# Kernel tuning notes

Measured on AMD Instinct MI355X. Metric: run time of the kernel, lower is better.

Reference implementation:

```python
import jax, jax.numpy as jnp
import numpy as np

N_HEAD = 16
N_FEAT = 1024
D_K = N_FEAT // N_HEAD
BATCH = 8
SEQ = 1024
LN_EPS = 1e-5
MIN_VAL = float(np.finfo(np.float32).min)


def setup_inputs() -> dict:
    key = jax.random.key(0)
    ks = jax.random.split(key, 8)
    s = 0.02  # small init scale for weights to keep activations sane
    return {
        "x": jax.random.normal(ks[0], (BATCH, SEQ, N_FEAT), jnp.float32),
        "pos_k": jax.random.normal(ks[1], (SEQ, SEQ, D_K), jnp.float32) * s,
        "mask": jnp.ones((BATCH, SEQ, SEQ), jnp.int32),
        "ln_scale": jnp.ones((N_FEAT,), jnp.float32),
        "ln_bias": jnp.zeros((N_FEAT,), jnp.float32),
        "wq": jax.random.normal(ks[2], (N_FEAT, N_FEAT), jnp.float32) * s,
        "bq": jnp.zeros((N_FEAT,), jnp.float32),
        "wk": jax.random.normal(ks[3], (N_FEAT, N_FEAT), jnp.float32) * s,
        "bk": jnp.zeros((N_FEAT,), jnp.float32),
        "wv": jax.random.normal(ks[4], (N_FEAT, N_FEAT), jnp.float32) * s,
        "bv": jnp.zeros((N_FEAT,), jnp.float32),
        "wo": jax.random.normal(ks[5], (N_FEAT, N_FEAT), jnp.float32) * s,
        "bo": jnp.zeros((N_FEAT,), jnp.float32),
    }


def reference(x, pos_k, mask, ln_scale, ln_bias, wq, bq, wk, bk, wv, bv, wo, bo):
    b, t, f = x.shape
    h, d = N_HEAD, D_K
    # LayerNorm over feature dim
    mu = jnp.mean(x, axis=-1, keepdims=True)
    var = jnp.mean((x - mu) ** 2, axis=-1, keepdims=True)
    xn = (x - mu) / jnp.sqrt(var + LN_EPS) * ln_scale + ln_bias
    # QKV projections (torch Linear: y = x @ W^T + b), split heads -> (b, h, t, d)
    q = (xn @ wq.T + bq).reshape(b, t, h, d).transpose(0, 2, 1, 3)
    k = (xn @ wk.T + bk).reshape(b, t, h, d).transpose(0, 2, 1, 3)
    v = (xn @ wv.T + bv).reshape(b, t, h, d).transpose(0, 2, 1, 3)
    # content score A and relative-position score B
    A = jnp.einsum("bhtd,bhsd->bhts", q, k)
    B = jnp.einsum("bhtd,tsd->bhts", q, pos_k)
    scores = (A + B) / jnp.sqrt(jnp.asarray(d, scores_dtype := x.dtype))
    m = (mask[:, None, :, :] == 0)  # (b, 1, t, s) broadcast over heads
    scores = jnp.where(m, MIN_VAL, scores)
    attn = jax.nn.softmax(scores, axis=-1)
    attn = jnp.where(m, 0.0, attn)
    out = jnp.einsum("bhts,bhsd->bhtd", attn, v)
    out = out.transpose(0, 2, 1, 3).reshape(b, t, h * d)
    return out @ wo.T + bo
```

## Files before the change

kernel.cpp:

```cpp
#include <hip/hip_runtime.h>
#include <hip/hip_bf16.h>

typedef unsigned short ushort_t;
typedef short short8 __attribute__((ext_vector_type(8)));
typedef unsigned short ushort8 __attribute__((ext_vector_type(8)));
typedef unsigned short ushortx4 __attribute__((ext_vector_type(4)));
typedef float fx4 __attribute__((ext_vector_type(4)));
typedef int ix4 __attribute__((ext_vector_type(4)));

#define MFMA(a, b, c) __builtin_amdgcn_mfma_f32_16x16x32_bf16((a), (b), (c), 0, 0, 0)

__device__ __forceinline__ ushort_t f2bf(float f) {
  __hip_bfloat16 h = __float2bfloat16(f);
  return *(ushort_t*)&h;
}
__device__ __forceinline__ float bf2f(ushort_t h) {
  union { unsigned u; float f; } c; c.u = ((unsigned)h) << 16;
  return c.f;
}
__device__ __forceinline__ void gload16(const ushort_t* g, ushort_t* l) {
  __builtin_amdgcn_global_load_lds((const __attribute__((address_space(1))) void*)g,
                                   (__attribute__((address_space(3))) void*)l, 16, 0, 0);
}

__global__ __launch_bounds__(256) void cvt4_kernel(const float* __restrict__ s0,
                                                   const float* __restrict__ s1,
                                                   const float* __restrict__ s2,
                                                   const float* __restrict__ s3,
                                                   ushort_t* __restrict__ d0,
                                                   ushort_t* __restrict__ d1,
                                                   ushort_t* __restrict__ d2,
                                                   ushort_t* __restrict__ d3) {
  int bi = blockIdx.x;
  const float* src = (bi < 1024) ? s0 : (bi < 2048) ? s1 : (bi < 3072) ? s2 : s3;
  ushort_t* dst = (bi < 1024) ? d0 : (bi < 2048) ? d1 : (bi < 3072) ? d2 : d3;
  int i = (bi & 1023) * 256 + threadIdx.x;
  fx4 v = *(const fx4*)&src[(size_t)i * 4];
  ushortx4 o;
#pragma unroll
  for (int j = 0; j < 4; ++j) o[j] = f2bf(v[j]);
  *(ushortx4*)&dst[(size_t)i * 4] = o;
}

__global__ __launch_bounds__(256) void ln_kernel(const float* __restrict__ x,
                                                 const float* __restrict__ sc,
                                                 const float* __restrict__ bi,
                                                 ushort_t* __restrict__ xn) {
  __shared__ float red[8];
  int row = blockIdx.x, tid = threadIdx.x;
  const float* xr = x + (size_t)row * 1024;
  fx4 v = *(const fx4*)&xr[tid * 4];
  float s = v[0] + v[1] + v[2] + v[3];
  float s2 = v[0] * v[0] + v[1] * v[1] + v[2] * v[2] + v[3] * v[3];
#pragma unroll
  for (int m = 32; m >= 1; m >>= 1) {
    s += __shfl_xor(s, m);
    s2 += __shfl_xor(s2, m);
  }
  int wave = tid >> 6;
  if ((tid & 63) == 0) { red[wave * 2] = s; red[wave * 2 + 1] = s2; }
  __syncthreads();
  s = red[0] + red[2] + red[4] + red[6];
  s2 = red[1] + red[3] + red[5] + red[7];
  float mu = s * (1.f / 1024.f);
  float var = s2 * (1.f / 1024.f) - mu * mu;
  float rs = rsqrtf(var + 1e-5f);
  fx4 scv = *(const fx4*)&sc[tid * 4];
  fx4 biv = *(const fx4*)&bi[tid * 4];
  ushortx4 o;
#pragma unroll
  for (int j = 0; j < 4; ++j) o[j] = f2bf((v[j] - mu) * rs * scv[j] + biv[j]);
  *(ushortx4*)&xn[(size_t)row * 1024 + tid * 4] = o;
}

__global__ __launch_bounds__(256) void maskpack_kernel(const int* __restrict__ mask,
                                                       unsigned* __restrict__ bits) {
  __shared__ unsigned char nib[256];
  int row = blockIdx.x, tid = threadIdx.x;
  ix4 m = *(const ix4*)&mask[(size_t)row * 1024 + tid * 4];
  nib[tid] = (unsigned char)((m[0] != 0 ? 1 : 0) | (m[1] != 0 ? 2 : 0) |
                             (m[2] != 0 ? 4 : 0) | (m[3] != 0 ? 8 : 0));
  __syncthreads();
  if (tid < 32) {
    unsigned w = 0;
#pragma unroll
    for (int j = 0; j < 8; ++j) w |= ((unsigned)nib[tid * 8 + j]) << (j * 4);
    bits[(size_t)row * 32 + tid] = w;
  }
}

template <int F32OUT>
__global__ __launch_bounds__(256) void gemm_bt(const ushort_t* __restrict__ A,
                                               const ushort_t* __restrict__ B,
                                               const float* __restrict__ bias, void* C,
                                               int M, int N, int K) {
  __shared__ ushort_t lA[4096];
  __shared__ ushort_t lB[4096];
  int bm = blockIdx.y * 128, bn = blockIdx.x * 128;
  int tid = threadIdx.x;
  int wave = tid >> 6, lane = tid & 63;
  int wm = (wave >> 1) * 64, wn = (wave & 1) * 64;
  int l15 = lane & 15, lg = lane >> 4;
  int r0 = tid >> 2, c0 = (tid & 3) * 8;
  int g1 = 256 + tid, r1 = g1 >> 2, c1 = (g1 & 3) * 8;
  int lb0 = (wave * 64) * 8;
  int lb1 = (256 + wave * 64) * 8;
  fx4 acc[4][4] = {};
  for (int k0 = 0; k0 < K; k0 += 32) {
    __syncthreads();
    gload16(&A[(size_t)(bm + r0) * K + k0 + c0], &lA[lb0]);
    gload16(&A[(size_t)(bm + r1) * K + k0 + c1], &lA[lb1]);
    gload16(&B[(size_t)(bn + r0) * K + k0 + c0], &lB[lb0]);
    gload16(&B[(size_t)(bn + r1) * K + k0 + c1], &lB[lb1]);
    __syncthreads();
    short8 af[4], bf[4];
#pragma unroll
    for (int i = 0; i < 4; ++i) af[i] = *(const short8*)&lA[(wm + i * 16 + l15) * 32 + lg * 8];
#pragma unroll
    for (int i = 0; i < 4; ++i) bf[i] = *(const short8*)&lB[(wn + i * 16 + l15) * 32 + lg * 8];
#pragma unroll
    for (int i = 0; i < 4; ++i)
#pragma unroll
      for (int j = 0; j < 4; ++j) acc[i][j] = MFMA(af[i], bf[j], acc[i][j]);
  }
#pragma unroll
  for (int j = 0; j < 4; ++j) {
    int n = bn + wn + j * 16 + l15;
    float bv = bias[n];
#pragma unroll
    for (int i = 0; i < 4; ++i) {
      int mr = bm + wm + i * 16 + lg * 4;
#pragma unroll
      for (int r = 0; r < 4; ++r) {
        float val = acc[i][j][r] + bv;
        if (F32OUT)
          ((float*)C)[(size_t)(mr + r) * N + n] = val;
        else
          ((ushort_t*)C)[(size_t)(mr + r) * N + n] = f2bf(val);
      }
    }
  }
}

__device__ __forceinline__ void loadset(const float* base, int c, fx4* r) {
  const float* p = base + (size_t)c * 1024;
  r[0] = *(const fx4*)p;
  r[1] = *(const fx4*)(p + 4);
  r[2] = *(const fx4*)(p + 32);
  r[3] = *(const fx4*)(p + 36);
}
__device__ __forceinline__ void cvtset(const fx4* r, short8& f0, short8& f1) {
#pragma unroll
  for (int j = 0; j < 4; ++j) {
    f0[j] = (short)f2bf(r[0][j]); f0[j + 4] = (short)f2bf(r[1][j]);
    f1[j] = (short)f2bf(r[2][j]); f1[j + 4] = (short)f2bf(r[3][j]);
  }
}

__global__ __launch_bounds__(256, 3) void ball_kernel(const ushort_t* __restrict__ q,
                                                      const float* __restrict__ pos_k,
                                                      ushort_t* __restrict__ B_all) {
  __shared__ ushort_t lq[128 * 64];
  int t = blockIdx.y, sx = blockIdx.x;
  int tid = threadIdx.x, wave = tid >> 6, lane = tid & 63, l15 = lane & 15, lg = lane >> 4;
  const float* pk = pos_k + (size_t)t * 65536;
  int sw = sx * 512 + wave * 128;
  const float* base = pk + (size_t)(sw + l15) * 64 + lg * 8;

  fx4 raw[4][4];
#pragma unroll
  for (int c = 0; c < 4; ++c) loadset(base, c, raw[c]);

#pragma unroll
  for (int it = 0; it < 4; ++it) {
    int u = tid + it * 256;
    int row = u >> 3, cu = u & 7;
    ushort8 vv = *(const ushort8*)&q[((size_t)((row >> 4) * 1024 + t)) * 1024 + (row & 15) * 64 + cu * 8];
    *(ushort8*)&lq[(row * 128 + ((cu * 16) ^ ((row & 7) << 4))) >> 1] = vv;
  }
  __syncthreads();

  short8 af0[4], af1[4];
#pragma unroll
  for (int c = 0; c < 4; ++c) cvtset(raw[c], af0[c], af1[c]);

#pragma unroll
  for (int g = 0; g < 2; ++g) {
    if (g == 0) {
#pragma unroll
      for (int c = 0; c < 4; ++c) loadset(base, 4 + c, raw[c]);
    }
    __builtin_amdgcn_sched_barrier(0);
#pragma unroll
    for (int j = 0; j < 8; ++j) {
      int row_ = j * 16 + l15;
      int cb_ = (row_ & 7) << 4;
      short8 q0 = *(const short8*)&lq[(row_ * 128 + ((lg * 16) ^ cb_)) >> 1];
      short8 q1 = *(const short8*)&lq[(row_ * 128 + ((64 + lg * 16) ^ cb_)) >> 1];
      fx4 z = {};
      size_t rb = ((size_t)row_ << 20) + (size_t)t * 1024 + (size_t)(sw + g * 64);
#pragma unroll
      for (int c = 0; c < 4; ++c) {
        fx4 a = MFMA(af0[c], q0, z);
        a = MFMA(af1[c], q1, a);
        ushortx4 o;
#pragma unroll
        for (int r = 0; r < 4; ++r) o[r] = f2bf(a[r]);
        *(ushortx4*)&B_all[rb + c * 16 + lg * 4] = o;
      }
    }
    __builtin_amdgcn_sched_barrier(0);
    if (g == 0) {
#pragma unroll
      for (int c = 0; c < 4; ++c) cvtset(raw[c], af0[c], af1[c]);
    }
  }
}

__global__ __launch_bounds__(256) void attn_kernel(const ushort_t* __restrict__ q,
                                                   const ushort_t* __restrict__ k,
                                                   const ushort_t* __restrict__ v,
                                                   const ushort_t* __restrict__ B_all,
                                                   const unsigned* __restrict__ mbits,
                                                   ushort_t* __restrict__ out) {
  __shared__ ushort_t lK[64][72];
  __shared__ ushort_t lVt[64][72];
  __shared__ ushort_t lP[4][16][72];
  int bh = blockIdx.y, b = bh >> 4, h = bh & 15;
  int t0 = blockIdx.x * 64;
  int tid = threadIdx.x, wave = tid >> 6, lane = tid & 63, l15 = lane & 15, lg = lane >> 4;
  int tw = t0 + wave * 16;
  short8 qf[2];
#pragma unroll
  for (int ks = 0; ks < 2; ++ks)
    qf[ks] = *(const short8*)&q[((size_t)(b * 1024 + tw + l15)) * 1024 + h * 64 + ks * 32 + lg * 8];
  fx4 o[4] = {};
  float mrun = -INFINITY, lsum = 0.f;
  int trow = tw + l15;
  const unsigned* mrow = &mbits[((size_t)b * 1024 + trow) * 32];
  size_t ballrow = ((size_t)bh * 1024 + trow) * 1024;

  int rs = tid >> 3, c8g = tid & 7, c8 = c8g * 8;
  const ushort_t* kbase = &k[((size_t)(b * 1024) + rs) * 1024 + h * 64 + c8];
  const ushort_t* vbase = &v[((size_t)(b * 1024) + rs) * 1024 + h * 64 + c8];
  ushort8 kr0 = *(const ushort8*)(kbase);
  ushort8 kr1 = *(const ushort8*)(kbase + 32 * 1024);
  ushort8 vr0 = *(const ushort8*)(vbase);
  ushort8 vr1 = *(const ushort8*)(vbase + 32 * 1024);
  int vs0 = (rs + 8 * c8g) & 63;
  int vs1 = (rs + 32 + 8 * c8g) & 63;

  for (int s0 = 0; s0 < 1024; s0 += 64) {
    __syncthreads();
    *(ushort8*)&lK[rs][c8] = kr0;
    *(ushort8*)&lK[rs + 32][c8] = kr1;
#pragma unroll
    for (int j = 0; j < 8; ++j) {
      lVt[c8 + j][vs0] = vr0[j];
      lVt[c8 + j][vs1] = vr1[j];
    }
    __syncthreads();
    if (s0 + 64 < 1024) {
      size_t off = (size_t)(s0 + 64) * 1024;
      kr0 = *(const ushort8*)(kbase + off);
      kr1 = *(const ushort8*)(kbase + off + 32 * 1024);
      vr0 = *(const ushort8*)(vbase + off);
      vr1 = *(const ushort8*)(vbase + off + 32 * 1024);
    }
    __builtin_amdgcn_sched_barrier(0);
    ushortx4 b4[4];
#pragma unroll
    for (int mf = 0; mf < 4; ++mf)
      b4[mf] = *(const ushortx4*)&B_all[ballrow + s0 + mf * 16 + lg * 4];
    uint2 mw = *(const uint2*)&mrow[s0 >> 5];
    unsigned long long wb = ((unsigned long long)mw.y << 32) | mw.x;
    __builtin_amdgcn_sched_barrier(0);
    fx4 st[4];
#pragma unroll
    for (int mf = 0; mf < 4; ++mf) {
      fx4 c4 = {};
#pragma unroll
      for (int ks = 0; ks < 2; ++ks) {
        short8 kf = *(const short8*)&lK[mf * 16 + l15][ks * 32 + lg * 8];
        c4 = MFMA(kf, qf[ks], c4);
      }
      st[mf] = c4;
    }
    float p[16];
    float mt = -INFINITY;
#pragma unroll
    for (int mf = 0; mf < 4; ++mf) {
#pragma unroll
      for (int r = 0; r < 4; ++r) {
        float sv = (st[mf][r] + bf2f(b4[mf][r])) * 0.125f;
        int sl = mf * 16 + lg * 4 + r;
        if (!((wb >> sl) & 1ull)) sv = -INFINITY;
        p[mf * 4 + r] = sv;
        mt = fmaxf(mt, sv);
      }
    }
    mt = fmaxf(mt, __shfl_xor(mt, 16));
    mt = fmaxf(mt, __shfl_xor(mt, 32));
    float mnew = fmaxf(mrun, mt);
    float alpha = (mnew == -INFINITY) ? 1.f : __expf(mrun - mnew);
    mrun = mnew;
    float ps = 0.f;
#pragma unroll
    for (int i = 0; i < 16; ++i) {
      float pv = (mnew == -INFINITY) ? 0.f : __expf(p[i] - mnew);
      p[i] = pv;
      ps += pv;
    }
    ps += __shfl_xor(ps, 16);
    ps += __shfl_xor(ps, 32);
    lsum = lsum * alpha + ps;
#pragma unroll
    for (int mf = 0; mf < 4; ++mf) {
      ushortx4 pk4;
#pragma unroll
      for (int r = 0; r < 4; ++r) pk4[r] = f2bf(p[mf * 4 + r]);
      *(ushortx4*)&lP[wave][l15][mf * 16 + lg * 4] = pk4;
    }
    float aw[4];
#pragma unroll
    for (int r = 0; r < 4; ++r) aw[r] = __shfl(alpha, lg * 4 + r);
#pragma unroll
    for (int nf = 0; nf < 4; ++nf)
#pragma unroll
      for (int r = 0; r < 4; ++r) o[nf][r] *= aw[r];
#pragma unroll
    for (int ks = 0; ks < 2; ++ks) {
      short8 pf = *(const short8*)&lP[wave][l15][ks * 32 + lg * 8];
#pragma unroll
      for (int nf = 0; nf < 4; ++nf) {
        int d_ = nf * 16 + l15;
        int sb_ = (ks * 32 + lg * 8 + 8 * (d_ >> 3)) & 63;
        short8 vf = *(const short8*)&lVt[d_][sb_];
        o[nf] = MFMA(pf, vf, o[nf]);
      }
    }
  }
  float rl = (lsum > 0.f) ? 1.f / lsum : 0.f;
  float rw[4];
#pragma unroll
  for (int r = 0; r < 4; ++r) rw[r] = __shfl(rl, lg * 4 + r);
#pragma unroll
  for (int nf = 0; nf < 4; ++nf)
#pragma unroll
    for (int r = 0; r < 4; ++r) {
      float val = o[nf][r] * rw[r];
      out[((size_t)(b * 1024 + tw + lg * 4 + r)) * 1024 + h * 64 + nf * 16 + l15] = f2bf(val);
    }
}

extern "C" void kernel_launch(void* const* d_in, const int* in_sizes, int n_in, void* d_out,
                              int out_size, void* d_ws, size_t ws_size, hipStream_t stream) {
  (void)in_sizes; (void)n_in; (void)out_size; (void)ws_size;
  const float* x = (const float*)d_in[0];
  const float* pos_k = (const float*)d_in[1];
  const int* mask = (const int*)d_in[2];
  const float* ln_scale = (const float*)d_in[3];
  const float* ln_bias = (const float*)d_in[4];
  const float* wq = (const float*)d_in[5];
  const float* bq = (const float*)d_in[6];
  const float* wk = (const float*)d_in[7];
  const float* bk = (const float*)d_in[8];
  const float* wv = (const float*)d_in[9];
  const float* bv = (const float*)d_in[10];
  const float* wo = (const float*)d_in[11];
  const float* bo = (const float*)d_in[12];
  float* out = (float*)d_out;
  char* ws = (char*)d_ws;
  const size_t MB = 1ull << 20;
  ushort_t* xn = (ushort_t*)(ws + 0 * MB);
  ushort_t* qb = (ushort_t*)(ws + 16 * MB);
  ushort_t* kb = (ushort_t*)(ws + 32 * MB);
  ushort_t* vb = (ushort_t*)(ws + 48 * MB);
  ushort_t* ao = (ushort_t*)(ws + 64 * MB);
  ushort_t* wqb = (ushort_t*)(ws + 80 * MB);
  ushort_t* wkb = (ushort_t*)(ws + 82 * MB);
  ushort_t* wvb = (ushort_t*)(ws + 84 * MB);
  ushort_t* wob = (ushort_t*)(ws + 86 * MB);
  ushort_t* ball = (ushort_t*)(ws + 88 * MB);
  unsigned* mbits = (unsigned*)(ws + 0 * MB);

  cvt4_kernel<<<4096, 256, 0, stream>>>(wq, wk, wv, wo, wqb, wkb, wvb, wob);
  ln_kernel<<<8192, 256, 0, stream>>>(x, ln_scale, ln_bias, xn);
  dim3 gg(8, 64);
  gemm_bt<0><<<gg, 256, 0, stream>>>(xn, wqb, bq, qb, 8192, 1024, 1024);
  gemm_bt<0><<<gg, 256, 0, stream>>>(xn, wkb, bk, kb, 8192, 1024, 1024);
  gemm_bt<0><<<gg, 256, 0, stream>>>(xn, wvb, bv, vb, 8192, 1024, 1024);
  maskpack_kernel<<<8192, 256, 0, stream>>>(mask, mbits);
  ball_kernel<<<dim3(2, 1024), 256, 0, stream>>>(qb, pos_k, ball);
  attn_kernel<<<dim3(16, 128), 256, 0, stream>>>(qb, kb, vb, ball, mbits, ao);
  gemm_bt<1><<<gg, 256, 0, stream>>>(ao, wob, bo, out, 8192, 1024, 1024);
}
```

Measured before the change: 436.1 us.

## Fold softmax scale into Q projection, use exp2, skip mask and rescale when possible

Q is pre-scaled in the projection epilogue by 1/sqrt(d)*log2(e), so attention scores feed exp2 directly and the per-element scale multiply disappears. Because ball is built from the scaled q, the positional term carries the same scale. Masking is skipped when the whole wave's tile is unmasked, and the online-softmax rescale of the output accumulators is skipped when the running max did not grow. V transpose stores pack two values per 32-bit write, the P tile in LDS uses an XOR swizzle instead of padding, and K/V pointers advance incrementally. The extra wave votes add branches, and bf16 rounding of pre-scaled q slightly changes numerics.

```diff
diff --git a/kernel.cpp b/kernel.cpp
--- a/kernel.cpp
+++ b/kernel.cpp
@@ -7,8 +7,11 @@
 typedef unsigned short ushortx4 __attribute__((ext_vector_type(4)));
 typedef float fx4 __attribute__((ext_vector_type(4)));
 typedef int ix4 __attribute__((ext_vector_type(4)));
+typedef unsigned uint2v __attribute__((ext_vector_type(2)));
 
 #define MFMA(a, b, c) __builtin_amdgcn_mfma_f32_16x16x32_bf16((a), (b), (c), 0, 0, 0)
+
+#define QSCALE 0.18033688011112042f
 
 __device__ __forceinline__ ushort_t f2bf(float f) {
   __hip_bfloat16 h = __float2bfloat16(f);
@@ -93,7 +96,7 @@
 __global__ __launch_bounds__(256) void gemm_bt(const ushort_t* __restrict__ A,
                                                const ushort_t* __restrict__ B,
                                                const float* __restrict__ bias, void* C,
-                                               int M, int N, int K) {
+                                               int M, int N, int K, float oscale) {
   __shared__ ushort_t lA[4096];
   __shared__ ushort_t lB[4096];
   int bm = blockIdx.y * 128, bn = blockIdx.x * 128;
@@ -132,7 +135,7 @@
       int mr = bm + wm + i * 16 + lg * 4;
 #pragma unroll
       for (int r = 0; r < 4; ++r) {
-        float val = acc[i][j][r] + bv;
+        float val = (acc[i][j][r] + bv) * oscale;
         if (F32OUT)
           ((float*)C)[(size_t)(mr + r) * N + n] = val;
         else
@@ -224,8 +227,8 @@
                                                    const unsigned* __restrict__ mbits,
                                                    ushort_t* __restrict__ out) {
   __shared__ ushort_t lK[64][72];
-  __shared__ ushort_t lVt[64][72];
-  __shared__ ushort_t lP[4][16][72];
+  __shared__ ushort_t lVt[64 * 72];
+  __shared__ ushort_t lP[4 * 16 * 64];
   int bh = blockIdx.y, b = bh >> 4, h = bh & 15;
   int t0 = blockIdx.x * 64;
   int tid = threadIdx.x, wave = tid >> 6, lane = tid & 63, l15 = lane & 15, lg = lane >> 4;
@@ -240,33 +243,35 @@
   const unsigned* mrow = &mbits[((size_t)b * 1024 + trow) * 32];
   size_t ballrow = ((size_t)bh * 1024 + trow) * 1024;
 
-  int rs = tid >> 3, c8g = tid & 7, c8 = c8g * 8;
-  const ushort_t* kbase = &k[((size_t)(b * 1024) + rs) * 1024 + h * 64 + c8];
-  const ushort_t* vbase = &v[((size_t)(b * 1024) + rs) * 1024 + h * 64 + c8];
+  int rsv = tid >> 3, c8g = tid & 7, c8 = c8g * 8;
+  const ushort_t* kbase = &k[((size_t)(b * 1024) + rsv) * 1024 + h * 64 + c8];
+  const ushort_t* vbase = &v[((size_t)(b * 1024) + 2 * rsv) * 1024 + h * 64 + c8];
   ushort8 kr0 = *(const ushort8*)(kbase);
   ushort8 kr1 = *(const ushort8*)(kbase + 32 * 1024);
   ushort8 vr0 = *(const ushort8*)(vbase);
-  ushort8 vr1 = *(const ushort8*)(vbase + 32 * 1024);
-  int vs0 = (rs + 8 * c8g) & 63;
-  int vs1 = (rs + 32 + 8 * c8g) & 63;
+  ushort8 vr1 = *(const ushort8*)(vbase + 1024);
+  int vslot = (2 * rsv + 8 * c8g) & 63;
+  int lpw = wave * 1024 + l15 * 64;
+  int lpx = (l15 & 7) << 4;
 
   for (int s0 = 0; s0 < 1024; s0 += 64) {
     __syncthreads();
-    *(ushort8*)&lK[rs][c8] = kr0;
-    *(ushort8*)&lK[rs + 32][c8] = kr1;
+    *(ushort8*)&lK[rsv][c8] = kr0;
+    *(ushort8*)&lK[rsv + 32][c8] = kr1;
 #pragma unroll
     for (int j = 0; j < 8; ++j) {
-      lVt[c8 + j][vs0] = vr0[j];
-      lVt[c8 + j][vs1] = vr1[j];
+      unsigned w = (unsigned)vr0[j] | ((unsigned)vr1[j] << 16);
+      *(unsigned*)&lVt[(c8 + j) * 72 + vslot] = w;
     }
     __syncthreads();
     if (s0 + 64 < 1024) {
-      size_t off = (size_t)(s0 + 64) * 1024;
-      kr0 = *(const ushort8*)(kbase + off);
-      kr1 = *(const ushort8*)(kbase + off + 32 * 1024);
-      vr0 = *(const ushort8*)(vbase + off);
-      vr1 = *(const ushort8*)(vbase + off + 32 * 1024);
-    }
+      kr0 = *(const ushort8*)(kbase + 65536);
+      kr1 = *(const ushort8*)(kbase + 65536 + 32 * 1024);
+      vr0 = *(const ushort8*)(vbase + 65536);
+      vr1 = *(const ushort8*)(vbase + 65536 + 1024);
+    }
+    kbase += 65536;
+    vbase += 65536;
     __builtin_amdgcn_sched_barrier(0);
     ushortx4 b4[4];
 #pragma unroll
@@ -275,7 +280,7 @@
     uint2 mw = *(const uint2*)&mrow[s0 >> 5];
     unsigned long long wb = ((unsigned long long)mw.y << 32) | mw.x;
     __builtin_amdgcn_sched_barrier(0);
-    fx4 st[4];
+    float p[16];
 #pragma unroll
     for (int mf = 0; mf < 4; ++mf) {
       fx4 c4 = {};
@@ -284,58 +289,71 @@
         short8 kf = *(const short8*)&lK[mf * 16 + l15][ks * 32 + lg * 8];
         c4 = MFMA(kf, qf[ks], c4);
       }
-      st[mf] = c4;
-    }
-    float p[16];
-    float mt = -INFINITY;
-#pragma unroll
-    for (int mf = 0; mf < 4; ++mf) {
-#pragma unroll
-      for (int r = 0; r < 4; ++r) {
-        float sv = (st[mf][r] + bf2f(b4[mf][r])) * 0.125f;
-        int sl = mf * 16 + lg * 4 + r;
-        if (!((wb >> sl) & 1ull)) sv = -INFINITY;
-        p[mf * 4 + r] = sv;
-        mt = fmaxf(mt, sv);
-      }
-    }
+#pragma unroll
+      for (int r = 0; r < 4; ++r) p[mf * 4 + r] = c4[r] + bf2f(b4[mf][r]);
+    }
+    if (!__all(wb == ~0ull)) {
+#pragma unroll
+      for (int i = 0; i < 16; ++i) {
+        int sl = (i >> 2) * 16 + lg * 4 + (i & 3);
+        if (!((wb >> sl) & 1ull)) p[i] = -INFINITY;
+      }
+    }
+    float m0 = fmaxf(p[0], p[1]), m1 = fmaxf(p[2], p[3]);
+    float m2 = fmaxf(p[4], p[5]), m3 = fmaxf(p[6], p[7]);
+    float m4 = fmaxf(p[8], p[9]), m5 = fmaxf(p[10], p[11]);
+    float m6 = fmaxf(p[12], p[13]), m7 = fmaxf(p[14], p[15]);
+    m0 = fmaxf(m0, m1); m2 = fmaxf(m2, m3); m4 = fmaxf(m4, m5); m6 = fmaxf(m6, m7);
+    float mt = fmaxf(fmaxf(m0, m2), fmaxf(m4, m6));
     mt = fmaxf(mt, __shfl_xor(mt, 16));
     mt = fmaxf(mt, __shfl_xor(mt, 32));
-    float mnew = fmaxf(mrun, mt);
-    float alpha = (mnew == -INFINITY) ? 1.f : __expf(mrun - mnew);
-    mrun = mnew;
     float ps = 0.f;
-#pragma unroll
-    for (int i = 0; i < 16; ++i) {
-      float pv = (mnew == -INFINITY) ? 0.f : __expf(p[i] - mnew);
-      p[i] = pv;
-      ps += pv;
-    }
-    ps += __shfl_xor(ps, 16);
-    ps += __shfl_xor(ps, 32);
-    lsum = lsum * alpha + ps;
+    if (__all((mt <= mrun) && (mrun != -INFINITY))) {
+#pragma unroll
+      for (int i = 0; i < 16; ++i) {
+        float pv = exp2f(p[i] - mrun);
+        p[i] = pv;
+        ps += pv;
+      }
+      ps += __shfl_xor(ps, 16);
+      ps += __shfl_xor(ps, 32);
+      lsum += ps;
+    } else {
+      float mnew = fmaxf(mrun, mt);
+      float alpha = (mnew == -INFINITY) ? 1.f : exp2f(mrun - mnew);
+      mrun = mnew;
+#pragma unroll
+      for (int i = 0; i < 16; ++i) {
+        float pv = (mnew == -INFINITY) ? 0.f : exp2f(p[i] - mnew);
+        p[i] = pv;
+        ps += pv;
+      }
+      ps += __shfl_xor(ps, 16);
+      ps += __shfl_xor(ps, 32);
+      lsum = lsum * alpha + ps;
+      float aw[4];
+#pragma unroll
+      for (int r = 0; r < 4; ++r) aw[r] = __shfl(alpha, lg * 4 + r);
+#pragma unroll
+      for (int nf = 0; nf < 4; ++nf)
+#pragma unroll
+        for (int r = 0; r < 4; ++r) o[nf][r] *= aw[r];
+    }
 #pragma unroll
     for (int mf = 0; mf < 4; ++mf) {
-      ushortx4 pk4;
-#pragma unroll
-      for (int r = 0; r < 4; ++r) pk4[r] = f2bf(p[mf * 4 + r]);
-      *(ushortx4*)&lP[wave][l15][mf * 16 + lg * 4] = pk4;
-    }
-    float aw[4];
-#pragma unroll
-    for (int r = 0; r < 4; ++r) aw[r] = __shfl(alpha, lg * 4 + r);
-#pragma unroll
-    for (int nf = 0; nf < 4; ++nf)
-#pragma unroll
-      for (int r = 0; r < 4; ++r) o[nf][r] *= aw[r];
+      unsigned w0 = (unsigned)f2bf(p[mf * 4 + 0]) | ((unsigned)f2bf(p[mf * 4 + 1]) << 16);
+      unsigned w1 = (unsigned)f2bf(p[mf * 4 + 2]) | ((unsigned)f2bf(p[mf * 4 + 3]) << 16);
+      uint2v wv; wv[0] = w0; wv[1] = w1;
+      *(uint2v*)&lP[lpw + (((mf * 32 + lg * 8) ^ lpx) >> 1)] = wv;
+    }
 #pragma unroll
     for (int ks = 0; ks < 2; ++ks) {
-      short8 pf = *(const short8*)&lP[wave][l15][ks * 32 + lg * 8];
+      short8 pf = *(const short8*)&lP[lpw + (((ks * 64 + lg * 16) ^ lpx) >> 1)];
 #pragma unroll
       for (int nf = 0; nf < 4; ++nf) {
         int d_ = nf * 16 + l15;
         int sb_ = (ks * 32 + lg * 8 + 8 * (d_ >> 3)) & 63;
-        short8 vf = *(const short8*)&lVt[d_][sb_];
+        short8 vf = *(const short8*)&lVt[d_ * 72 + sb_];
         o[nf] = MFMA(pf, vf, o[nf]);
       }
     }
@@ -387,11 +405,11 @@
   cvt4_kernel<<<4096, 256, 0, stream>>>(wq, wk, wv, wo, wqb, wkb, wvb, wob);
   ln_kernel<<<8192, 256, 0, stream>>>(x, ln_scale, ln_bias, xn);
   dim3 gg(8, 64);
-  gemm_bt<0><<<gg, 256, 0, stream>>>(xn, wqb, bq, qb, 8192, 1024, 1024);
-  gemm_bt<0><<<gg, 256, 0, stream>>>(xn, wkb, bk, kb, 8192, 1024, 1024);
-  gemm_bt<0><<<gg, 256, 0, stream>>>(xn, wvb, bv, vb, 8192, 1024, 1024);
+  gemm_bt<0><<<gg, 256, 0, stream>>>(xn, wqb, bq, qb, 8192, 1024, 1024, QSCALE);
+  gemm_bt<0><<<gg, 256, 0, stream>>>(xn, wkb, bk, kb, 8192, 1024, 1024, 1.f);
+  gemm_bt<0><<<gg, 256, 0, stream>>>(xn, wvb, bv, vb, 8192, 1024, 1024, 1.f);
   maskpack_kernel<<<8192, 256, 0, stream>>>(mask, mbits);
   ball_kernel<<<dim3(2, 1024), 256, 0, stream>>>(qb, pos_k, ball);
   attn_kernel<<<dim3(16, 128), 256, 0, stream>>>(qb, kb, vb, ball, mbits, ao);
-  gemm_bt<1><<<gg, 256, 0, stream>>>(ao, wob, bo, out, 8192, 1024, 1024);
-}
+  gemm_bt<1><<<gg, 256, 0, stream>>>(ao, wob, bo, out, 8192, 1024, 1024, 1.f);
+}
```

Result: slower. 470.0 us (+7.8%).
